# Optimization experiments

Measured on AMD Instinct MI355X. Metric: run time of the kernel, lower is better.

## Reference

```python
import jax, jax.numpy as jnp
import numpy as np
import math

B, N, C = 1, 2048, 256
H, CH = 8, 32
PQ, PV = 8, 12
CZ = 32
BQ, BK = 32, 128
NB = N // BQ
PAD = (BK - BQ) // 2
INF = 1e8
EPS = 1e-8

_KIDX = np.arange(NB)[:, None] * BQ + np.arange(BK)[None, :] - PAD
_KVALID = (_KIDX >= 0) & (_KIDX < N)
_KIDX_C = np.clip(_KIDX, 0, N - 1)


def _quat_to_rot(q):
    q = q / jnp.linalg.norm(q, axis=-1, keepdims=True)
    w, x, y, z = q[..., 0], q[..., 1], q[..., 2], q[..., 3]
    return jnp.stack([
        jnp.stack([1 - 2 * (y * y + z * z), 2 * (x * y - w * z), 2 * (x * z + w * y)], -1),
        jnp.stack([2 * (x * y + w * z), 1 - 2 * (x * x + z * z), 2 * (y * z - w * x)], -1),
        jnp.stack([2 * (x * z - w * y), 2 * (y * z + w * x), 1 - 2 * (x * x + y * y)], -1)], -2)


def _to_queries(x):
    # [B, N, ...] -> [B, NB, BQ, ...]
    return x.reshape((B, NB, BQ) + x.shape[2:])


def _to_keys(x):
    # [B, N, ...] -> [B, NB, BK, ...] zero-padded sliding key windows
    g = x[:, _KIDX_C]
    v = jnp.asarray(_KVALID, x.dtype).reshape((1, NB, BK) + (1,) * (x.ndim - 2))
    return g * v


def _ln(x):
    m = x.mean(-1, keepdims=True)
    var = x.var(-1, keepdims=True)
    return (x - m) / jnp.sqrt(var + 1e-5)


def setup_inputs():
    key = jax.random.key(0)
    ks = jax.random.split(key, 16)
    p = 0.02
    return {
        's': jax.random.normal(ks[0], (B, N, C), jnp.float32),
        'cond': jax.random.normal(ks[1], (B, N, C), jnp.float32),
        'z': jax.random.normal(ks[2], (B, NB, BQ, BK, CZ), jnp.float32),
        'trans': jax.random.normal(ks[3], (B, N, 3), jnp.float32),
        'rots': _quat_to_rot(jax.random.normal(ks[4], (B, N, 4), jnp.float32)),
        's_mask': jnp.ones((B, N), jnp.float32),
        'Wq': jax.random.normal(ks[5], (C, H * CH)) * p,
        'Wk': jax.random.normal(ks[6], (C, H * CH)) * p,
        'Wv': jax.random.normal(ks[7], (C, H * CH)) * p,
        'Wqp': jax.random.normal(ks[8], (C, H * PQ * 3)) * p,
        'Wkvp': jax.random.normal(ks[9], (C, H * (PQ + PV) * 3)) * p,
        'Wb': jax.random.normal(ks[10], (CZ, H)) * p,
        'Wdz': jax.random.normal(ks[11], (CZ, CZ // 4)) * p,
        'head_weights': jnp.full((H,), 0.5413),
        'Wout': jax.random.normal(ks[12], (H * (CZ // 4 + CH + PV * 4), C)) * p,
        'Wg': jax.random.normal(ks[13], (C, C)) * p,
        'bg': jnp.zeros((C,)),
        'Wbeta': jax.random.normal(ks[14], (C, C)) * p,
        'bbeta': jnp.zeros((C,)),
        'g_z': jnp.ones((CZ,)),
        'b_z': jnp.zeros((CZ,)),
    }


def reference(s, cond, z, trans, rots, s_mask, Wq, Wk, Wv, Wqp, Wkvp, Wb, Wdz,
              head_weights, Wout, Wg, bg, Wbeta, bbeta, g_z, b_z):
    # AdaLN on s conditioned on cond; LayerNorm on z
    s = _ln(s) * (cond @ Wg + bg) + (cond @ Wbeta + bbeta)
    z = _ln(z) * g_z + b_z

    q_in = _to_queries(s)            # [B,NB,BQ,C]
    k_in = _to_keys(s)               # [B,NB,BK,C]
    q_t = _to_queries(trans)         # [B,NB,BQ,3]
    q_R = _to_queries(rots)          # [B,NB,BQ,3,3]
    k_t = _to_keys(trans)
    k_R = _to_keys(rots)
    # zero-padded key rotations -> identity
    zero = jnp.all(k_R == 0, axis=(-2, -1))[..., None, None]
    k_R = jnp.where(zero, jnp.eye(3, dtype=k_R.dtype), k_R)

    q = (q_in @ Wq).reshape(B, NB, BQ, H, CH)
    k = (k_in @ Wk).reshape(B, NB, BK, H, CH)
    v = (k_in @ Wv).reshape(B, NB, BK, H, CH)

    q_pts = (q_in @ Wqp).reshape(B, NB, BQ, H * PQ, 3)
    q_pts = jnp.einsum('bnqij,bnqpj->bnqpi', q_R, q_pts) + q_t[..., None, :]
    q_pts = q_pts.reshape(B, NB, BQ, H, PQ, 3)

    kv_pts = (k_in @ Wkvp).reshape(B, NB, BK, H * (PQ + PV), 3)
    kv_pts = jnp.einsum('bnkij,bnkpj->bnkpi', k_R, kv_pts) + k_t[..., None, :]
    kv_pts = kv_pts.reshape(B, NB, BK, H, PQ + PV, 3)
    k_pts, v_pts = kv_pts[..., :PQ, :], kv_pts[..., PQ:, :]

    b = z @ Wb                                    # [B,NB,BQ,BK,H]
    a = jnp.einsum('bnqhc,bnkhc->bnqkh', q, k) * math.sqrt(1.0 / (3 * CH))
    a = a + math.sqrt(1.0 / 3.0) * b

    disp = q_pts[:, :, :, None] - k_pts[:, :, None]   # [B,NB,BQ,BK,H,PQ,3]
    d2 = jnp.sum(disp * disp, axis=-1)                # [B,NB,BQ,BK,H,PQ]
    hw = jax.nn.softplus(head_weights) * math.sqrt(1.0 / (3 * (PQ * 9.0 / 2)))
    pt_att = -0.5 * jnp.sum(d2 * hw[:, None], axis=-1)   # [B,NB,BQ,BK,H]

    m_q = _to_queries(s_mask[..., None])              # [B,NB,BQ,1]
    m_k = _to_keys(s_mask[..., None])                 # [B,NB,BK,1]
    attn_mask = m_q * jnp.swapaxes(m_k, -1, -2)       # [B,NB,BQ,BK]
    attn_mask = INF * (attn_mask - 1.0)

    a = a + pt_att + attn_mask[..., None]
    a = jnp.swapaxes(a, -1, -2)                       # [B,NB,BQ,H,BK]
    a = jax.nn.softmax(a, axis=-1)

    o = jnp.einsum('bnqhk,bnkhc->bnqhc', a, v).reshape(B, NB, BQ, H * CH)
    o_pt = jnp.einsum('bnqhk,bnkhvc->bnqhvc', a, v_pts)      # [B,NB,BQ,H,PV,3]
    o_pt = jnp.einsum('bnqji,bnqhvj->bnqhvi', q_R,
                      o_pt - q_t[:, :, :, None, None, :])     # invert apply
    o_pt_norm = jnp.sqrt(jnp.sum(o_pt ** 2, -1) + EPS).reshape(B, NB, BQ, H * PV)
    o_pt = o_pt.reshape(B, NB, BQ, H * PV * 3)
    pair_z = z @ Wdz                                          # [B,NB,BQ,BK,CZ//4]
    o_pair = jnp.einsum('bnqhk,bnqkc->bnqhc', a, pair_z).reshape(B, NB, BQ, H * (CZ // 4))

    out = jnp.concatenate([o, o_pt, o_pt_norm, o_pair], -1) @ Wout
    return out.reshape(B, N, C)
```

## Files before the change

### kernel.cpp

```cpp
#include <hip/hip_runtime.h>
#include <hip/hip_bf16.h>
#include <math.h>

typedef __hip_bfloat16 bf16;
typedef __attribute__((ext_vector_type(8))) short short8;
typedef __attribute__((ext_vector_type(4))) float f32x4;

#define NRES 2048
#define CDIM 256
#define PADK 48
#define POS 1440

static __device__ __forceinline__ float b2f(bf16 x) { return __bfloat162float(x); }

static __device__ __forceinline__ bool flag_f32(const void* smask) {
    return *(const unsigned int*)smask == 0x3F800000u;
}
static __device__ __forceinline__ float dual_load(const void* p, size_t i, bool f32) {
    float vf = ((const float*)p)[f32 ? i : 0];
    float vb = b2f(((const bf16*)p)[f32 ? (size_t)0 : i]);
    return f32 ? vf : vb;
}

struct TransTable {
    const void* src[8];
    bf16* dst[8];
    int srcN[8];
    int nOff[8];
    int dstStride[8];
    int tileOff[9];
};
__global__ __launch_bounds__(256) void k_trans(TransTable tb, const void* __restrict__ smask) {
    bool f32 = flag_f32(smask);
    int b = blockIdx.x;
    int s = 0;
    while (b >= tb.tileOff[s + 1]) ++s;
    int rel = b - tb.tileOff[s];
    int ntTiles = tb.srcN[s] >> 5;
    int kt = rel / ntTiles, nt = rel % ntTiles;
    const void* src = tb.src[s];
    int srcN = tb.srcN[s];
    __shared__ float tile[32][33];
    int tx = threadIdx.x & 31, ty = threadIdx.x >> 5;
#pragma unroll
    for (int r = 0; r < 4; ++r) {
        int srow = kt * 32 + ty + r * 8;
        int scol = nt * 32 + tx;
        tile[ty + r * 8][tx] = dual_load(src, (size_t)srow * srcN + scol, f32);
    }
    __syncthreads();
    bf16* dst = tb.dst[s];
#pragma unroll
    for (int r = 0; r < 4; ++r) {
        int n = nt * 32 + ty + r * 8 + tb.nOff[s];
        int k = kt * 32 + tx;
        dst[(size_t)n * tb.dstStride[s] + k] = __float2bfloat16(tile[tx][ty + r * 8]);
    }
}

__global__ __launch_bounds__(256) void k_cast(const void* __restrict__ src, bf16* __restrict__ dst,
                                              int n, const void* __restrict__ smask) {
    bool f32 = flag_f32(smask);
    for (int i = blockIdx.x * 256 + threadIdx.x; i < n; i += gridDim.x * 256)
        dst[i] = __float2bfloat16(dual_load(src, i, f32));
}

__global__ __launch_bounds__(256) void k_gemm(
    const bf16* __restrict__ A, const bf16* __restrict__ Bt, void* __restrict__ Cv,
    int M, int N, int K, int totalTiles, int out_mode, const void* __restrict__ smask)
{
    int wid = threadIdx.x >> 6, lane = threadIdx.x & 63;
    int tid = blockIdx.x * 4 + wid;
    if (tid >= totalTiles) return;
    int tiles_n = N >> 4;
    int mt = tid / tiles_n, nt = tid % tiles_n;
    int idx = lane & 15, quad = lane >> 4;
    const bf16* Ap = A + (size_t)(mt * 16 + idx) * K + quad * 8;
    const bf16* Bp = Bt + (size_t)(nt * 16 + idx) * K + quad * 8;
    f32x4 acc = {0.f, 0.f, 0.f, 0.f};
    for (int k = 0; k < K; k += 32) {
        short8 af = *(const short8*)(Ap + k);
        short8 bfv = *(const short8*)(Bp + k);
        acc = __builtin_amdgcn_mfma_f32_16x16x32_bf16(af, bfv, acc, 0, 0, 0);
    }
    int orow = mt * 16 + quad * 4;
    int ocol = nt * 16 + idx;
    if (out_mode == 0) {
        float* C = (float*)Cv;
#pragma unroll
        for (int r = 0; r < 4; ++r) C[(size_t)(orow + r) * N + ocol] = acc[r];
    } else {
        if (flag_f32(smask)) {
            float* C = (float*)Cv;
#pragma unroll
            for (int r = 0; r < 4; ++r) C[(size_t)(orow + r) * N + ocol] = acc[r];
        } else {
            bf16* C = (bf16*)Cv;
#pragma unroll
            for (int r = 0; r < 4; ++r) C[(size_t)(orow + r) * N + ocol] = __float2bfloat16(acc[r]);
        }
    }
}

__global__ __launch_bounds__(256) void k_gemm22(
    const bf16* __restrict__ A, const bf16* __restrict__ Bt, float* __restrict__ C,
    int N, int K, int totalWaves)
{
    int wid = threadIdx.x >> 6, lane = threadIdx.x & 63;
    int tid = blockIdx.x * 4 + wid;
    if (tid >= totalWaves) return;
    int tiles_n = N >> 5;
    int mt = tid / tiles_n, nt = tid % tiles_n;
    int idx = lane & 15, quad = lane >> 4;
    const bf16* Ap0 = A + (size_t)(mt * 32 + idx) * K + quad * 8;
    const bf16* Ap1 = Ap0 + (size_t)16 * K;
    const bf16* Bp0 = Bt + (size_t)(nt * 32 + idx) * K + quad * 8;
    const bf16* Bp1 = Bp0 + (size_t)16 * K;
    f32x4 a00 = {0,0,0,0}, a01 = {0,0,0,0}, a10 = {0,0,0,0}, a11 = {0,0,0,0};
    for (int k = 0; k < K; k += 32) {
        short8 af0 = *(const short8*)(Ap0 + k);
        short8 af1 = *(const short8*)(Ap1 + k);
        short8 bf0 = *(const short8*)(Bp0 + k);
        short8 bf1 = *(const short8*)(Bp1 + k);
        a00 = __builtin_amdgcn_mfma_f32_16x16x32_bf16(af0, bf0, a00, 0, 0, 0);
        a01 = __builtin_amdgcn_mfma_f32_16x16x32_bf16(af0, bf1, a01, 0, 0, 0);
        a10 = __builtin_amdgcn_mfma_f32_16x16x32_bf16(af1, bf0, a10, 0, 0, 0);
        a11 = __builtin_amdgcn_mfma_f32_16x16x32_bf16(af1, bf1, a11, 0, 0, 0);
    }
    int orow = mt * 32 + quad * 4;
    int ocol = nt * 32 + idx;
#pragma unroll
    for (int r = 0; r < 4; ++r) {
        C[(size_t)(orow + r) * N + ocol] = a00[r];
        C[(size_t)(orow + r) * N + ocol + 16] = a01[r];
        C[(size_t)(orow + r + 16) * N + ocol] = a10[r];
        C[(size_t)(orow + r + 16) * N + ocol + 16] = a11[r];
    }
}

__global__ __launch_bounds__(256) void k_mod2(
    const void* __restrict__ s, const float* __restrict__ GB,
    const void* __restrict__ bg, const void* __restrict__ bbeta,
    const void* __restrict__ smask, bf16* __restrict__ SQb)
{
    __shared__ float ls[8][CDIM];
    __shared__ float mrs[8][2];
    bool f32 = flag_f32(smask);
    int r0 = blockIdx.x * 8;
    int t = threadIdx.x;
    for (int i = t; i < 8 * CDIM; i += 256) {
        int r = i >> 8, c = i & 255;
        ls[r][c] = dual_load(s, (size_t)(r0 + r) * CDIM + c, f32);
    }
    __syncthreads();
    int wave = t >> 6, lane = t & 63;
    for (int rr = 0; rr < 2; ++rr) {
        int r = wave * 2 + rr;
        float sum = 0.f, sq = 0.f;
        for (int j = lane; j < CDIM; j += 64) { float v = ls[r][j]; sum += v; sq += v * v; }
        for (int off = 32; off; off >>= 1) { sum += __shfl_xor(sum, off); sq += __shfl_xor(sq, off); }
        if (lane == 0) {
            float m = sum / CDIM;
            float var = fmaxf(sq / CDIM - m * m, 0.f);
            mrs[r][0] = m; mrs[r][1] = rsqrtf(var + 1e-5f);
        }
    }
    __syncthreads();
    int c = t;
    float bgc = dual_load(bg, c, f32), bbc = dual_load(bbeta, c, f32);
#pragma unroll
    for (int r = 0; r < 8; ++r) {
        float xn = (ls[r][c] - mrs[r][0]) * mrs[r][1];
        float gv = GB[(size_t)(r0 + r) * 512 + c] + bgc;
        float bv = GB[(size_t)(r0 + r) * 512 + 256 + c] + bbc;
        SQb[(size_t)(r0 + r) * CDIM + c] = __float2bfloat16(xn * gv + bv);
    }
}

__global__ __launch_bounds__(256) void k_rotate(
    const float* __restrict__ PO,
    const void* __restrict__ rots, const void* __restrict__ trans,
    const void* __restrict__ smask,
    float* __restrict__ QP, float* __restrict__ KP, float* __restrict__ VP)
{
    int i = blockIdx.x;
    int t = threadIdx.x;
    bool f32 = flag_f32(smask);
    __shared__ float R[9], T[3];
    if (t < 9) R[t] = dual_load(rots, (size_t)i * 9 + t, f32);
    if (t < 3) T[t] = dual_load(trans, (size_t)i * 3 + t, f32);
    __syncthreads();
    const float* qp = PO + (size_t)i * POS + 768;
    const float* kvp = PO + (size_t)i * POS + 960;
    if (t < 64) {
        int p = t;
        float x = qp[p * 3 + 0], y = qp[p * 3 + 1], z = qp[p * 3 + 2];
#pragma unroll
        for (int d = 0; d < 3; ++d)
            QP[(size_t)i * 192 + p * 3 + d] = R[d * 3] * x + R[d * 3 + 1] * y + R[d * 3 + 2] * z + T[d];
    } else if (t < 224) {
        int pp = t - 64;
        int h = pp / 20, j = pp % 20;
        float x = kvp[pp * 3 + 0], y = kvp[pp * 3 + 1], z = kvp[pp * 3 + 2];
        float o[3];
#pragma unroll
        for (int d = 0; d < 3; ++d)
            o[d] = R[d * 3] * x + R[d * 3 + 1] * y + R[d * 3 + 2] * z + T[d];
        if (j < 8) {
#pragma unroll
            for (int d = 0; d < 3; ++d) KP[(size_t)i * 192 + (h * 8 + j) * 3 + d] = o[d];
        } else {
#pragma unroll
            for (int d = 0; d < 3; ++d) VP[(size_t)i * 288 + (h * 12 + (j - 8)) * 3 + d] = o[d];
        }
    }
}

__global__ __launch_bounds__(256) void k_z(
    const void* __restrict__ z, const void* __restrict__ Wb, const void* __restrict__ Wdz,
    const void* __restrict__ g_z, const void* __restrict__ b_z,
    const void* __restrict__ smask,
    float* __restrict__ Bz, float* __restrict__ PZ)
{
    __shared__ float wb[32][8], wdz[32][8], gz[32], bz[32];
    bool f32 = flag_f32(smask);
    int t = threadIdx.x;
    {
        int j = t >> 3, c = t & 7;
        wb[j][c] = dual_load(Wb, t, f32);
        wdz[j][c] = dual_load(Wdz, t, f32);
    }
    if (t < 32) { gz[t] = dual_load(g_z, t, f32); bz[t] = dual_load(b_z, t, f32); }
    __syncthreads();
    size_t r = (size_t)blockIdx.x * 256 + t;
    float zv[32];
    float sum = 0.f, sq = 0.f;
    if (f32) {
        const float4* zp = (const float4*)((const float*)z + r * 32);
#pragma unroll
        for (int j4 = 0; j4 < 8; ++j4) {
            float4 v4 = zp[j4];
            zv[j4 * 4 + 0] = v4.x; zv[j4 * 4 + 1] = v4.y; zv[j4 * 4 + 2] = v4.z; zv[j4 * 4 + 3] = v4.w;
        }
    } else {
        const bf16* zp = (const bf16*)z + r * 32;
#pragma unroll
        for (int j = 0; j < 32; ++j) zv[j] = b2f(zp[j]);
    }
#pragma unroll
    for (int j = 0; j < 32; ++j) { float v = zv[j]; sum += v; sq += v * v; }
    float m = sum / 32.f;
    float var = fmaxf(sq / 32.f - m * m, 0.f);
    float rstd = rsqrtf(var + 1e-5f);
#pragma unroll
    for (int j = 0; j < 32; ++j) zv[j] = (zv[j] - m) * rstd * gz[j] + bz[j];
    float bacc[8], pacc[8];
#pragma unroll
    for (int c = 0; c < 8; ++c) { bacc[c] = 0.f; pacc[c] = 0.f; }
    for (int j = 0; j < 32; ++j) {
        float v = zv[j];
#pragma unroll
        for (int c = 0; c < 8; ++c) { bacc[c] += v * wb[j][c]; pacc[c] += v * wdz[j][c]; }
    }
    int n = (int)(r >> 12);
    int q = (int)(r >> 7) & 31;
    int k = (int)r & 127;
#pragma unroll
    for (int h = 0; h < 8; ++h)
        Bz[(size_t)n * 32768 + (size_t)h * 4096 + q * 128 + k] = bacc[h];
#pragma unroll
    for (int c = 0; c < 8; ++c)
        PZ[(((size_t)(n * 32 + q)) * 8 + c) * 128 + k] = pacc[c];
}

__global__ __launch_bounds__(256) void k_attn_out(
    const float* __restrict__ PO,
    const float* __restrict__ QP, const float* __restrict__ KP, const float* __restrict__ VP,
    const float* __restrict__ Bz, const float* __restrict__ PZ,
    const void* __restrict__ rots, const void* __restrict__ trans,
    const void* __restrict__ smask, const void* __restrict__ head_weights,
    bf16* __restrict__ CATb)
{
    __shared__ char buf[70016];
    __shared__ float rowq[32], rowk[128], mk[128], mqv[32];
    bf16* Qf  = (bf16*)buf;
    bf16* Kf  = (bf16*)(buf + 4608);
    bf16* Vt  = (bf16*)(buf + 23040);
    bf16* As  = (bf16*)(buf + 44800);
    float* S  = (float*)(buf + 53504);
    float* OPT = (float*)(buf + 53504);

    const int n = blockIdx.x >> 3, h = blockIdx.x & 7;
    const int t = threadIdx.x;
    const bool f32 = flag_f32(smask);
    const int n32 = n * 32;

    float hwv = dual_load(head_weights, h, f32);
    float ptc = -0.5f * log1pf(expf(hwv)) * 0.09622504486493764f;
    float m2ptc = -2.f * ptc;
    const float qkscale = 0.10206207261596575f;
    const float bscale = 0.5773502691896258f;

    for (int i = t; i < 32 * 16; i += 256) {
        int q = i >> 4, g = i & 15;
        float4 v = {0.f, 0.f, 0.f, 0.f};
        int col;
        if (g < 8) { v = *(const float4*)(PO + (size_t)(n32 + q) * POS + h * 32 + g * 4); col = g * 4; }
        else if (g < 14) { v = *(const float4*)(QP + (size_t)(n32 + q) * 192 + h * 24 + (g - 8) * 4); col = 32 + (g - 8) * 4; }
        else col = 56 + (g - 14) * 4;
        bf16* wp = Qf + q * 72 + col;
        wp[0] = __float2bfloat16(v.x); wp[1] = __float2bfloat16(v.y);
        wp[2] = __float2bfloat16(v.z); wp[3] = __float2bfloat16(v.w);
    }
    for (int i = t; i < 128 * 16; i += 256) {
        int k = i >> 4, g = i & 15;
        int kg = n32 + k - PADK;
        bool valid = (kg >= 0 && kg < NRES);
        float4 v = {0.f, 0.f, 0.f, 0.f};
        int col;
        if (g < 8) {
            if (valid) {
                v = *(const float4*)(PO + (size_t)kg * POS + 256 + h * 32 + g * 4);
                v.x *= qkscale; v.y *= qkscale; v.z *= qkscale; v.w *= qkscale;
            }
            col = g * 4;
        } else if (g < 14) {
            if (valid) {
                v = *(const float4*)(KP + (size_t)kg * 192 + h * 24 + (g - 8) * 4);
                v.x *= m2ptc; v.y *= m2ptc; v.z *= m2ptc; v.w *= m2ptc;
            }
            col = 32 + (g - 8) * 4;
        } else col = 56 + (g - 14) * 4;
        bf16* wp = Kf + k * 72 + col;
        wp[0] = __float2bfloat16(v.x); wp[1] = __float2bfloat16(v.y);
        wp[2] = __float2bfloat16(v.z); wp[3] = __float2bfloat16(v.w);
    }
    for (int i = t; i < 128 * 17; i += 256) {
        int k = i / 17, g = i % 17;
        int kg = n32 + k - PADK;
        bool valid = (kg >= 0 && kg < NRES);
        float4 v = {0.f, 0.f, 0.f, 0.f};
        int x0;
        if (g < 8) {
            if (valid) v = *(const float4*)(PO + (size_t)kg * POS + 512 + h * 32 + g * 4);
            x0 = g * 4;
        } else {
            if (valid) v = *(const float4*)(VP + (size_t)kg * 288 + h * 36 + (g - 8) * 4);
            x0 = 32 + (g - 8) * 4;
        }
        Vt[(x0 + 0) * 136 + k] = __float2bfloat16(v.x);
        Vt[(x0 + 1) * 136 + k] = __float2bfloat16(v.y);
        Vt[(x0 + 2) * 136 + k] = __float2bfloat16(v.z);
        Vt[(x0 + 3) * 136 + k] = __float2bfloat16(v.w);
    }
    for (int i = t; i < 12 * 128; i += 256) {
        int x = 68 + (i >> 7), k = i & 127;
        Vt[x * 136 + k] = __float2bfloat16(0.f);
    }
    if (t < 32) {
        mqv[t] = dual_load(smask, n32 + t, f32);
        float s2 = 0.f;
#pragma unroll
        for (int j = 0; j < 24; ++j) {
            float v = QP[(size_t)(n32 + t) * 192 + h * 24 + j];
            s2 += v * v;
        }
        rowq[t] = ptc * s2;
    }
    if (t >= 128) {
        int k = t - 128;
        int kg = n32 + k - PADK;
        bool valid = (kg >= 0 && kg < NRES);
        float mv = 0.f, s2 = 0.f;
        if (valid) {
            mv = dual_load(smask, kg, f32);
#pragma unroll
            for (int j = 0; j < 24; ++j) {
                float v = KP[(size_t)kg * 192 + h * 24 + j];
                s2 += v * v;
            }
        }
        mk[k] = mv;
        rowk[k] = ptc * s2;
    }
    __syncthreads();

    const int wid = t >> 6, lane = t & 63, idx = lane & 15, quad = lane >> 4;
#pragma unroll
    for (int i = 0; i < 4; ++i) {
        int tt = wid * 4 + i;
        int mt = tt >> 3, nt = tt & 7;
        f32x4 acc = {0.f, 0.f, 0.f, 0.f};
#pragma unroll
        for (int kk = 0; kk < 2; ++kk) {
            short8 af  = *(const short8*)(Qf + (mt * 16 + idx) * 72 + kk * 32 + quad * 8);
            short8 bfv = *(const short8*)(Kf + (nt * 16 + idx) * 72 + kk * 32 + quad * 8);
            acc = __builtin_amdgcn_mfma_f32_16x16x32_bf16(af, bfv, acc, 0, 0, 0);
        }
#pragma unroll
        for (int r = 0; r < 4; ++r) {
            int q = mt * 16 + quad * 4 + r;
            int k = nt * 16 + idx;
            float bz = Bz[(size_t)n * 32768 + (size_t)h * 4096 + q * 128 + k];
            float msk = 1e8f * (mqv[q] * mk[k] - 1.f);
            S[q * 129 + k] = acc[r] + bscale * bz + rowq[q] + rowk[k] + msk;
        }
    }
    __syncthreads();

    for (int rr = 0; rr < 8; ++rr) {
        int q = wid * 8 + rr;
        float v0 = S[q * 129 + lane], v1 = S[q * 129 + lane + 64];
        float mx = fmaxf(v0, v1);
        for (int off = 32; off; off >>= 1) mx = fmaxf(mx, __shfl_xor(mx, off));
        float e0 = expf(v0 - mx), e1 = expf(v1 - mx);
        float sm = e0 + e1;
        for (int off = 32; off; off >>= 1) sm += __shfl_xor(sm, off);
        float inv = 1.f / sm;
        As[q * 136 + lane] = __float2bfloat16(e0 * inv);
        As[q * 136 + lane + 64] = __float2bfloat16(e1 * inv);
    }
    __syncthreads();

    {
        int q = t >> 3, c = t & 7;
        const float4* pzp = (const float4*)(PZ + (((size_t)(n32 + q)) * 8 + c) * 128);
        float acc = 0.f;
        for (int k4 = 0; k4 < 32; ++k4) {
            float4 pv = pzp[k4];
            int k = k4 * 4;
            acc += b2f(As[q * 136 + k + 0]) * pv.x + b2f(As[q * 136 + k + 1]) * pv.y
                 + b2f(As[q * 136 + k + 2]) * pv.z + b2f(As[q * 136 + k + 3]) * pv.w;
        }
        CATb[(size_t)(n32 + q) * 704 + 640 + h * 8 + c] = __float2bfloat16(acc);
    }
#pragma unroll
    for (int i = 0; i < 3; ++i) {
        int tt = wid + i * 4;
        if (tt >= 10) break;
        int mt = tt / 5, nt = tt % 5;
        f32x4 acc = {0.f, 0.f, 0.f, 0.f};
#pragma unroll
        for (int kk = 0; kk < 4; ++kk) {
            short8 af  = *(const short8*)(As + (mt * 16 + idx) * 136 + kk * 32 + quad * 8);
            short8 bfv = *(const short8*)(Vt + (nt * 16 + idx) * 136 + kk * 32 + quad * 8);
            acc = __builtin_amdgcn_mfma_f32_16x16x32_bf16(af, bfv, acc, 0, 0, 0);
        }
        int x = nt * 16 + idx;
#pragma unroll
        for (int r = 0; r < 4; ++r) {
            int q = mt * 16 + quad * 4 + r;
            if (x < 32)
                CATb[(size_t)(n32 + q) * 704 + h * 32 + x] = __float2bfloat16(acc[r]);
            else if (x < 68)
                OPT[q * 37 + (x - 32)] = acc[r];
        }
    }
    __syncthreads();

    for (int i = t; i < 32 * 12; i += 256) {
        int q = i / 12, v = i % 12;
        int g = n32 + q;
        float R[9], T[3];
#pragma unroll
        for (int d = 0; d < 9; ++d) R[d] = dual_load(rots, (size_t)g * 9 + d, f32);
#pragma unroll
        for (int d = 0; d < 3; ++d) T[d] = dual_load(trans, (size_t)g * 3 + d, f32);
        float x = OPT[q * 37 + v * 3 + 0] - T[0];
        float y = OPT[q * 37 + v * 3 + 1] - T[1];
        float z = OPT[q * 37 + v * 3 + 2] - T[2];
        float o0 = R[0] * x + R[3] * y + R[6] * z;
        float o1 = R[1] * x + R[4] * y + R[7] * z;
        float o2 = R[2] * x + R[5] * y + R[8] * z;
        size_t cb = (size_t)g * 704;
        CATb[cb + 256 + (h * 12 + v) * 3 + 0] = __float2bfloat16(o0);
        CATb[cb + 256 + (h * 12 + v) * 3 + 1] = __float2bfloat16(o1);
        CATb[cb + 256 + (h * 12 + v) * 3 + 2] = __float2bfloat16(o2);
        CATb[cb + 544 + h * 12 + v] = __float2bfloat16(sqrtf(o0 * o0 + o1 * o1 + o2 * o2 + 1e-8f));
    }
}

extern "C" void kernel_launch(void* const* d_in, const int* in_sizes, int n_in,
                              void* d_out, int out_size, void* d_ws, size_t ws_size,
                              hipStream_t stream) {
    const void* s       = d_in[0];
    const void* cond    = d_in[1];
    const void* z       = d_in[2];
    const void* trans   = d_in[3];
    const void* rots    = d_in[4];
    const void* s_mask  = d_in[5];
    const void* Wq      = d_in[6];
    const void* Wk      = d_in[7];
    const void* Wv      = d_in[8];
    const void* Wqp     = d_in[9];
    const void* Wkvp    = d_in[10];
    const void* Wb      = d_in[11];
    const void* Wdz     = d_in[12];
    const void* hweights= d_in[13];
    const void* Wout    = d_in[14];
    const void* Wg      = d_in[15];
    const void* bg      = d_in[16];
    const void* Wbeta   = d_in[17];
    const void* bbeta   = d_in[18];
    const void* g_z     = d_in[19];
    const void* b_z     = d_in[20];

    float* ws = (float*)d_ws;
    float* PO   = ws;
    float* GB   = PO + 2949120;
    float* QP   = GB + 1048576;
    float* KP   = QP + 393216;
    float* VP   = KP + 393216;
    float* Bz   = VP + 589824;
    float* PZ   = Bz + 2097152;
    float* fb   = PZ + 2097152;
    bf16* SQb   = (bf16*)fb;
    bf16* condb = (bf16*)(fb + 262144);
    bf16* CATb  = (bf16*)(fb + 524288);
    bf16* PWt   = (bf16*)(fb + 1245184);
    bf16* GWt   = (bf16*)(fb + 1429504);
    bf16* FWt   = (bf16*)(fb + 1495040);

    TransTable tb;
    tb.src[0] = Wq;   tb.dst[0] = PWt; tb.srcN[0] = 256; tb.nOff[0] = 0;   tb.dstStride[0] = 256;
    tb.src[1] = Wk;   tb.dst[1] = PWt; tb.srcN[1] = 256; tb.nOff[1] = 256; tb.dstStride[1] = 256;
    tb.src[2] = Wv;   tb.dst[2] = PWt; tb.srcN[2] = 256; tb.nOff[2] = 512; tb.dstStride[2] = 256;
    tb.src[3] = Wqp;  tb.dst[3] = PWt; tb.srcN[3] = 192; tb.nOff[3] = 768; tb.dstStride[3] = 256;
    tb.src[4] = Wkvp; tb.dst[4] = PWt; tb.srcN[4] = 480; tb.nOff[4] = 960; tb.dstStride[4] = 256;
    tb.src[5] = Wg;   tb.dst[5] = GWt; tb.srcN[5] = 256; tb.nOff[5] = 0;   tb.dstStride[5] = 256;
    tb.src[6] = Wbeta;tb.dst[6] = GWt; tb.srcN[6] = 256; tb.nOff[6] = 256; tb.dstStride[6] = 256;
    tb.src[7] = Wout; tb.dst[7] = FWt; tb.srcN[7] = 256; tb.nOff[7] = 0;   tb.dstStride[7] = 704;
    int tc[8] = {64, 64, 64, 48, 120, 64, 64, 176};
    tb.tileOff[0] = 0;
    for (int i = 0; i < 8; ++i) tb.tileOff[i + 1] = tb.tileOff[i] + tc[i];

    dim3 blk(256);
    k_trans<<<dim3(664), blk, 0, stream>>>(tb, s_mask);
    k_cast<<<dim3(256), blk, 0, stream>>>(cond, condb, NRES * CDIM, s_mask);
    k_gemm<<<dim3(1024), blk, 0, stream>>>(condb, GWt, GB, 2048, 512, 256, 4096, 0, s_mask);
    k_mod2<<<dim3(256), blk, 0, stream>>>(s, GB, bg, bbeta, s_mask, SQb);
    k_gemm22<<<dim3(720), blk, 0, stream>>>(SQb, PWt, PO, 1440, 256, 2880);
    k_rotate<<<dim3(NRES), blk, 0, stream>>>(PO, rots, trans, s_mask, QP, KP, VP);
    k_z<<<dim3(1024), blk, 0, stream>>>(z, Wb, Wdz, g_z, b_z, s_mask, Bz, PZ);
    k_attn_out<<<dim3(512), blk, 0, stream>>>(PO, QP, KP, VP, Bz, PZ, rots, trans, s_mask, hweights, CATb);
    k_gemm<<<dim3(512), blk, 0, stream>>>(CATb, FWt, d_out, 2048, 256, 704, 2048, 1, s_mask);
}
```

Measured before the change: 199.7 us.

## Fuse prep kernels, fold scales into weights, and store intermediates as bf16

Merges the weight transposes, the cond cast and the s layernorm into one prep launch. It fuses the gamma/beta GEMM with the modulation epilogue, and folds the qk and bias scales into the weights. The projection output and the pair-bias/pair-z intermediates are now stored as bf16, and the separate rotate kernel is removed so points are handled inside attention. This cuts the launch count and halves intermediate memory traffic, at the cost of extra bf16 rounding on intermediates.

```diff
diff --git a/kernel.cpp b/kernel.cpp
--- a/kernel.cpp
+++ b/kernel.cpp
@@ -12,7 +12,13 @@
 #define POS 1440
 
 static __device__ __forceinline__ float b2f(bf16 x) { return __bfloat162float(x); }
-
+static __device__ __forceinline__ float us2f(short u) {
+    return __uint_as_float(((unsigned)(unsigned short)u) << 16);
+}
+static __device__ __forceinline__ short f2s(float f) {
+    bf16 h = __float2bfloat16(f);
+    return *reinterpret_cast<short*>(&h);
+}
 static __device__ __forceinline__ bool flag_f32(const void* smask) {
     return *(const unsigned int*)smask == 0x3F800000u;
 }
@@ -22,88 +28,117 @@
     return f32 ? vf : vb;
 }
 
-struct TransTable {
+struct PrepTable {
     const void* src[8];
     bf16* dst[8];
     int srcN[8];
     int nOff[8];
     int dstStride[8];
+    float scl[8];
     int tileOff[9];
+    const void* s;
+    const void* cond;
+    bf16* condb;
+    bf16* xnb;
 };
-__global__ __launch_bounds__(256) void k_trans(TransTable tb, const void* __restrict__ smask) {
+__global__ __launch_bounds__(256) void k_prep(PrepTable tb, const void* __restrict__ smask) {
     bool f32 = flag_f32(smask);
     int b = blockIdx.x;
-    int s = 0;
-    while (b >= tb.tileOff[s + 1]) ++s;
-    int rel = b - tb.tileOff[s];
-    int ntTiles = tb.srcN[s] >> 5;
-    int kt = rel / ntTiles, nt = rel % ntTiles;
-    const void* src = tb.src[s];
-    int srcN = tb.srcN[s];
-    __shared__ float tile[32][33];
-    int tx = threadIdx.x & 31, ty = threadIdx.x >> 5;
-#pragma unroll
-    for (int r = 0; r < 4; ++r) {
-        int srow = kt * 32 + ty + r * 8;
-        int scol = nt * 32 + tx;
-        tile[ty + r * 8][tx] = dual_load(src, (size_t)srow * srcN + scol, f32);
-    }
-    __syncthreads();
-    bf16* dst = tb.dst[s];
-#pragma unroll
-    for (int r = 0; r < 4; ++r) {
-        int n = nt * 32 + ty + r * 8 + tb.nOff[s];
-        int k = kt * 32 + tx;
-        dst[(size_t)n * tb.dstStride[s] + k] = __float2bfloat16(tile[tx][ty + r * 8]);
-    }
-}
-
-__global__ __launch_bounds__(256) void k_cast(const void* __restrict__ src, bf16* __restrict__ dst,
-                                              int n, const void* __restrict__ smask) {
+    int t = threadIdx.x;
+    if (b < tb.tileOff[8]) {
+        int s = 0;
+        while (b >= tb.tileOff[s + 1]) ++s;
+        int rel = b - tb.tileOff[s];
+        int ntTiles = tb.srcN[s] >> 5;
+        int kt = rel / ntTiles, nt = rel % ntTiles;
+        const void* src = tb.src[s];
+        int srcN = tb.srcN[s];
+        float scl = tb.scl[s];
+        __shared__ float tile[32][33];
+        int tx = t & 31, ty = t >> 5;
+#pragma unroll
+        for (int r = 0; r < 4; ++r) {
+            int srow = kt * 32 + ty + r * 8;
+            int scol = nt * 32 + tx;
+            tile[ty + r * 8][tx] = dual_load(src, (size_t)srow * srcN + scol, f32);
+        }
+        __syncthreads();
+        bf16* dst = tb.dst[s];
+#pragma unroll
+        for (int r = 0; r < 4; ++r) {
+            int n = nt * 32 + ty + r * 8 + tb.nOff[s];
+            int k = kt * 32 + tx;
+            dst[(size_t)n * tb.dstStride[s] + k] = __float2bfloat16(tile[tx][ty + r * 8] * scl);
+        }
+        return;
+    }
+    b -= tb.tileOff[8];
+    if (b < 256) {
+        int i0 = b * 2048;
+        for (int i = t; i < 2048; i += 256)
+            tb.condb[i0 + i] = __float2bfloat16(dual_load(tb.cond, (size_t)(i0 + i), f32));
+        return;
+    }
+    b -= 256;
+    __shared__ float ls[8][CDIM];
+    __shared__ float mrs[8][2];
+    int r0 = b * 8;
+    for (int i = t; i < 8 * CDIM; i += 256) {
+        int r = i >> 8, c = i & 255;
+        ls[r][c] = dual_load(tb.s, (size_t)(r0 + r) * CDIM + c, f32);
+    }
+    __syncthreads();
+    int wave = t >> 6, lane = t & 63;
+    for (int rr = 0; rr < 2; ++rr) {
+        int r = wave * 2 + rr;
+        float sum = 0.f, sq = 0.f;
+        for (int j = lane; j < CDIM; j += 64) { float v = ls[r][j]; sum += v; sq += v * v; }
+        for (int off = 32; off; off >>= 1) { sum += __shfl_xor(sum, off); sq += __shfl_xor(sq, off); }
+        if (lane == 0) {
+            float m = sum / CDIM;
+            float var = fmaxf(sq / CDIM - m * m, 0.f);
+            mrs[r][0] = m; mrs[r][1] = rsqrtf(var + 1e-5f);
+        }
+    }
+    __syncthreads();
+    int c = t;
+#pragma unroll
+    for (int r = 0; r < 8; ++r)
+        tb.xnb[(size_t)(r0 + r) * CDIM + c] = __float2bfloat16((ls[r][c] - mrs[r][0]) * mrs[r][1]);
+}
+
+__global__ __launch_bounds__(256) void k_gb(
+    const bf16* __restrict__ condb, const bf16* __restrict__ GWt, const bf16* __restrict__ xnb,
+    const void* __restrict__ bg, const void* __restrict__ bbeta,
+    const void* __restrict__ smask, bf16* __restrict__ SQb)
+{
     bool f32 = flag_f32(smask);
-    for (int i = blockIdx.x * 256 + threadIdx.x; i < n; i += gridDim.x * 256)
-        dst[i] = __float2bfloat16(dual_load(src, i, f32));
-}
-
-__global__ __launch_bounds__(256) void k_gemm(
-    const bf16* __restrict__ A, const bf16* __restrict__ Bt, void* __restrict__ Cv,
-    int M, int N, int K, int totalTiles, int out_mode, const void* __restrict__ smask)
-{
     int wid = threadIdx.x >> 6, lane = threadIdx.x & 63;
     int tid = blockIdx.x * 4 + wid;
-    if (tid >= totalTiles) return;
-    int tiles_n = N >> 4;
-    int mt = tid / tiles_n, nt = tid % tiles_n;
+    int mt = tid >> 4, nt = tid & 15;
     int idx = lane & 15, quad = lane >> 4;
-    const bf16* Ap = A + (size_t)(mt * 16 + idx) * K + quad * 8;
-    const bf16* Bp = Bt + (size_t)(nt * 16 + idx) * K + quad * 8;
-    f32x4 acc = {0.f, 0.f, 0.f, 0.f};
-    for (int k = 0; k < K; k += 32) {
+    const bf16* Ap = condb + (size_t)(mt * 16 + idx) * 256 + quad * 8;
+    const bf16* B0 = GWt + (size_t)(nt * 16 + idx) * 256 + quad * 8;
+    const bf16* B1 = GWt + (size_t)(256 + nt * 16 + idx) * 256 + quad * 8;
+    f32x4 a0 = {0,0,0,0}, a1 = {0,0,0,0};
+    for (int k = 0; k < 256; k += 32) {
         short8 af = *(const short8*)(Ap + k);
-        short8 bfv = *(const short8*)(Bp + k);
-        acc = __builtin_amdgcn_mfma_f32_16x16x32_bf16(af, bfv, acc, 0, 0, 0);
-    }
+        a0 = __builtin_amdgcn_mfma_f32_16x16x32_bf16(af, *(const short8*)(B0 + k), a0, 0, 0, 0);
+        a1 = __builtin_amdgcn_mfma_f32_16x16x32_bf16(af, *(const short8*)(B1 + k), a1, 0, 0, 0);
+    }
+    int ocol = nt * 16 + idx;
+    float bgc = dual_load(bg, ocol, f32), bbc = dual_load(bbeta, ocol, f32);
     int orow = mt * 16 + quad * 4;
-    int ocol = nt * 16 + idx;
-    if (out_mode == 0) {
-        float* C = (float*)Cv;
-#pragma unroll
-        for (int r = 0; r < 4; ++r) C[(size_t)(orow + r) * N + ocol] = acc[r];
-    } else {
-        if (flag_f32(smask)) {
-            float* C = (float*)Cv;
-#pragma unroll
-            for (int r = 0; r < 4; ++r) C[(size_t)(orow + r) * N + ocol] = acc[r];
-        } else {
-            bf16* C = (bf16*)Cv;
-#pragma unroll
-            for (int r = 0; r < 4; ++r) C[(size_t)(orow + r) * N + ocol] = __float2bfloat16(acc[r]);
-        }
-    }
-}
-
-__global__ __launch_bounds__(256) void k_gemm22(
-    const bf16* __restrict__ A, const bf16* __restrict__ Bt, float* __restrict__ C,
+#pragma unroll
+    for (int r = 0; r < 4; ++r) {
+        int row = orow + r;
+        float xn = b2f(xnb[(size_t)row * 256 + ocol]);
+        SQb[(size_t)row * 256 + ocol] = __float2bfloat16(xn * (a0[r] + bgc) + (a1[r] + bbc));
+    }
+}
+
+__global__ __launch_bounds__(256) void k_gemm22b(
+    const bf16* __restrict__ A, const bf16* __restrict__ Bt, bf16* __restrict__ C,
     int N, int K, int totalWaves)
 {
     int wid = threadIdx.x >> 6, lane = threadIdx.x & 63;
@@ -131,88 +166,10 @@
     int ocol = nt * 32 + idx;
 #pragma unroll
     for (int r = 0; r < 4; ++r) {
-        C[(size_t)(orow + r) * N + ocol] = a00[r];
-        C[(size_t)(orow + r) * N + ocol + 16] = a01[r];
-        C[(size_t)(orow + r + 16) * N + ocol] = a10[r];
-        C[(size_t)(orow + r + 16) * N + ocol + 16] = a11[r];
-    }
-}
-
-__global__ __launch_bounds__(256) void k_mod2(
-    const void* __restrict__ s, const float* __restrict__ GB,
-    const void* __restrict__ bg, const void* __restrict__ bbeta,
-    const void* __restrict__ smask, bf16* __restrict__ SQb)
-{
-    __shared__ float ls[8][CDIM];
-    __shared__ float mrs[8][2];
-    bool f32 = flag_f32(smask);
-    int r0 = blockIdx.x * 8;
-    int t = threadIdx.x;
-    for (int i = t; i < 8 * CDIM; i += 256) {
-        int r = i >> 8, c = i & 255;
-        ls[r][c] = dual_load(s, (size_t)(r0 + r) * CDIM + c, f32);
-    }
-    __syncthreads();
-    int wave = t >> 6, lane = t & 63;
-    for (int rr = 0; rr < 2; ++rr) {
-        int r = wave * 2 + rr;
-        float sum = 0.f, sq = 0.f;
-        for (int j = lane; j < CDIM; j += 64) { float v = ls[r][j]; sum += v; sq += v * v; }
-        for (int off = 32; off; off >>= 1) { sum += __shfl_xor(sum, off); sq += __shfl_xor(sq, off); }
-        if (lane == 0) {
-            float m = sum / CDIM;
-            float var = fmaxf(sq / CDIM - m * m, 0.f);
-            mrs[r][0] = m; mrs[r][1] = rsqrtf(var + 1e-5f);
-        }
-    }
-    __syncthreads();
-    int c = t;
-    float bgc = dual_load(bg, c, f32), bbc = dual_load(bbeta, c, f32);
-#pragma unroll
-    for (int r = 0; r < 8; ++r) {
-        float xn = (ls[r][c] - mrs[r][0]) * mrs[r][1];
-        float gv = GB[(size_t)(r0 + r) * 512 + c] + bgc;
-        float bv = GB[(size_t)(r0 + r) * 512 + 256 + c] + bbc;
-        SQb[(size_t)(r0 + r) * CDIM + c] = __float2bfloat16(xn * gv + bv);
-    }
-}
-
-__global__ __launch_bounds__(256) void k_rotate(
-    const float* __restrict__ PO,
-    const void* __restrict__ rots, const void* __restrict__ trans,
-    const void* __restrict__ smask,
-    float* __restrict__ QP, float* __restrict__ KP, float* __restrict__ VP)
-{
-    int i = blockIdx.x;
-    int t = threadIdx.x;
-    bool f32 = flag_f32(smask);
-    __shared__ float R[9], T[3];
-    if (t < 9) R[t] = dual_load(rots, (size_t)i * 9 + t, f32);
-    if (t < 3) T[t] = dual_load(trans, (size_t)i * 3 + t, f32);
-    __syncthreads();
-    const float* qp = PO + (size_t)i * POS + 768;
-    const float* kvp = PO + (size_t)i * POS + 960;
-    if (t < 64) {
-        int p = t;
-        float x = qp[p * 3 + 0], y = qp[p * 3 + 1], z = qp[p * 3 + 2];
-#pragma unroll
-        for (int d = 0; d < 3; ++d)
-            QP[(size_t)i * 192 + p * 3 + d] = R[d * 3] * x + R[d * 3 + 1] * y + R[d * 3 + 2] * z + T[d];
-    } else if (t < 224) {
-        int pp = t - 64;
-        int h = pp / 20, j = pp % 20;
-        float x = kvp[pp * 3 + 0], y = kvp[pp * 3 + 1], z = kvp[pp * 3 + 2];
-        float o[3];
-#pragma unroll
-        for (int d = 0; d < 3; ++d)
-            o[d] = R[d * 3] * x + R[d * 3 + 1] * y + R[d * 3 + 2] * z + T[d];
-        if (j < 8) {
-#pragma unroll
-            for (int d = 0; d < 3; ++d) KP[(size_t)i * 192 + (h * 8 + j) * 3 + d] = o[d];
-        } else {
-#pragma unroll
-            for (int d = 0; d < 3; ++d) VP[(size_t)i * 288 + (h * 12 + (j - 8)) * 3 + d] = o[d];
-        }
+        C[(size_t)(orow + r) * N + ocol] = __float2bfloat16(a00[r]);
+        C[(size_t)(orow + r) * N + ocol + 16] = __float2bfloat16(a01[r]);
+        C[(size_t)(orow + r + 16) * N + ocol] = __float2bfloat16(a10[r]);
+        C[(size_t)(orow + r + 16) * N + ocol + 16] = __float2bfloat16(a11[r]);
     }
 }
 
@@ -220,14 +177,14 @@
     const void* __restrict__ z, const void* __restrict__ Wb, const void* __restrict__ Wdz,
     const void* __restrict__ g_z, const void* __restrict__ b_z,
     const void* __restrict__ smask,
-    float* __restrict__ Bz, float* __restrict__ PZ)
+    bf16* __restrict__ Bzb, bf16* __restrict__ PZb)
 {
     __shared__ float wb[32][8], wdz[32][8], gz[32], bz[32];
     bool f32 = flag_f32(smask);
     int t = threadIdx.x;
     {
         int j = t >> 3, c = t & 7;
-        wb[j][c] = dual_load(Wb, t, f32);
+        wb[j][c] = 0.5773502691896258f * dual_load(Wb, t, f32);
         wdz[j][c] = dual_load(Wdz, t, f32);
     }
     if (t < 32) { gz[t] = dual_load(g_z, t, f32); bz[t] = dual_load(b_z, t, f32); }
@@ -267,27 +224,26 @@
     int k = (int)r & 127;
 #pragma unroll
     for (int h = 0; h < 8; ++h)
-        Bz[(size_t)n * 32768 + (size_t)h * 4096 + q * 128 + k] = bacc[h];
+        Bzb[(size_t)n * 32768 + (size_t)h * 4096 + q * 128 + k] = __float2bfloat16(bacc[h]);
 #pragma unroll
     for (int c = 0; c < 8; ++c)
-        PZ[(((size_t)(n * 32 + q)) * 8 + c) * 128 + k] = pacc[c];
+        PZb[(((size_t)(n * 32 + q)) * 8 + c) * 128 + k] = __float2bfloat16(pacc[c]);
 }
 
 __global__ __launch_bounds__(256) void k_attn_out(
-    const float* __restrict__ PO,
-    const float* __restrict__ QP, const float* __restrict__ KP, const float* __restrict__ VP,
-    const float* __restrict__ Bz, const float* __restrict__ PZ,
+    const bf16* __restrict__ POb,
+    const bf16* __restrict__ Bzb, const bf16* __restrict__ PZb,
     const void* __restrict__ rots, const void* __restrict__ trans,
     const void* __restrict__ smask, const void* __restrict__ head_weights,
     bf16* __restrict__ CATb)
 {
     __shared__ char buf[70016];
     __shared__ float rowq[32], rowk[128], mk[128], mqv[32];
-    bf16* Qf  = (bf16*)buf;
-    bf16* Kf  = (bf16*)(buf + 4608);
-    bf16* Vt  = (bf16*)(buf + 23040);
-    bf16* As  = (bf16*)(buf + 44800);
-    float* S  = (float*)(buf + 53504);
+    short* QfS = (short*)buf;
+    short* KfS = (short*)(buf + 4608);
+    short* VtS = (short*)(buf + 23040);
+    short* AsS = (short*)(buf + 44800);
+    float* S   = (float*)(buf + 53504);
     float* OPT = (float*)(buf + 53504);
 
     const int n = blockIdx.x >> 3, h = blockIdx.x & 7;
@@ -298,90 +254,98 @@
     float hwv = dual_load(head_weights, h, f32);
     float ptc = -0.5f * log1pf(expf(hwv)) * 0.09622504486493764f;
     float m2ptc = -2.f * ptc;
-    const float qkscale = 0.10206207261596575f;
-    const float bscale = 0.5773502691896258f;
-
-    for (int i = t; i < 32 * 16; i += 256) {
-        int q = i >> 4, g = i & 15;
-        float4 v = {0.f, 0.f, 0.f, 0.f};
-        int col;
-        if (g < 8) { v = *(const float4*)(PO + (size_t)(n32 + q) * POS + h * 32 + g * 4); col = g * 4; }
-        else if (g < 14) { v = *(const float4*)(QP + (size_t)(n32 + q) * 192 + h * 24 + (g - 8) * 4); col = 32 + (g - 8) * 4; }
-        else col = 56 + (g - 14) * 4;
-        bf16* wp = Qf + q * 72 + col;
-        wp[0] = __float2bfloat16(v.x); wp[1] = __float2bfloat16(v.y);
-        wp[2] = __float2bfloat16(v.z); wp[3] = __float2bfloat16(v.w);
-    }
-    for (int i = t; i < 128 * 16; i += 256) {
-        int k = i >> 4, g = i & 15;
+    const short8 zero8 = {0,0,0,0,0,0,0,0};
+
+    if (t < 128) {
+        int q = t >> 2, g = t & 3;
+        *(short8*)(QfS + q * 72 + g * 8) =
+            *(const short8*)(POb + (size_t)(n32 + q) * POS + h * 32 + g * 8);
+    }
+    for (int i = t; i < 512; i += 256) {
+        int k = i >> 2, g = i & 3;
         int kg = n32 + k - PADK;
-        bool valid = (kg >= 0 && kg < NRES);
-        float4 v = {0.f, 0.f, 0.f, 0.f};
-        int col;
-        if (g < 8) {
-            if (valid) {
-                v = *(const float4*)(PO + (size_t)kg * POS + 256 + h * 32 + g * 4);
-                v.x *= qkscale; v.y *= qkscale; v.z *= qkscale; v.w *= qkscale;
-            }
-            col = g * 4;
-        } else if (g < 14) {
-            if (valid) {
-                v = *(const float4*)(KP + (size_t)kg * 192 + h * 24 + (g - 8) * 4);
-                v.x *= m2ptc; v.y *= m2ptc; v.z *= m2ptc; v.w *= m2ptc;
-            }
-            col = 32 + (g - 8) * 4;
-        } else col = 56 + (g - 14) * 4;
-        bf16* wp = Kf + k * 72 + col;
-        wp[0] = __float2bfloat16(v.x); wp[1] = __float2bfloat16(v.y);
-        wp[2] = __float2bfloat16(v.z); wp[3] = __float2bfloat16(v.w);
-    }
-    for (int i = t; i < 128 * 17; i += 256) {
-        int k = i / 17, g = i % 17;
+        short8 v = zero8;
+        if (kg >= 0 && kg < NRES)
+            v = *(const short8*)(POb + (size_t)kg * POS + 256 + h * 32 + g * 8);
+        *(short8*)(KfS + k * 72 + g * 8) = v;
+    }
+    for (int i = t; i < 512; i += 256) {
+        int k = i >> 2, g = i & 3;
         int kg = n32 + k - PADK;
-        bool valid = (kg >= 0 && kg < NRES);
-        float4 v = {0.f, 0.f, 0.f, 0.f};
-        int x0;
-        if (g < 8) {
-            if (valid) v = *(const float4*)(PO + (size_t)kg * POS + 512 + h * 32 + g * 4);
-            x0 = g * 4;
-        } else {
-            if (valid) v = *(const float4*)(VP + (size_t)kg * 288 + h * 36 + (g - 8) * 4);
-            x0 = 32 + (g - 8) * 4;
-        }
-        Vt[(x0 + 0) * 136 + k] = __float2bfloat16(v.x);
-        Vt[(x0 + 1) * 136 + k] = __float2bfloat16(v.y);
-        Vt[(x0 + 2) * 136 + k] = __float2bfloat16(v.z);
-        Vt[(x0 + 3) * 136 + k] = __float2bfloat16(v.w);
-    }
-    for (int i = t; i < 12 * 128; i += 256) {
-        int x = 68 + (i >> 7), k = i & 127;
-        Vt[x * 136 + k] = __float2bfloat16(0.f);
-    }
-    if (t < 32) {
-        mqv[t] = dual_load(smask, n32 + t, f32);
-        float s2 = 0.f;
-#pragma unroll
-        for (int j = 0; j < 24; ++j) {
-            float v = QP[(size_t)(n32 + t) * 192 + h * 24 + j];
-            s2 += v * v;
-        }
-        rowq[t] = ptc * s2;
-    }
-    if (t >= 128) {
-        int k = t - 128;
+        short8 v = zero8;
+        if (kg >= 0 && kg < NRES)
+            v = *(const short8*)(POb + (size_t)kg * POS + 512 + h * 32 + g * 8);
+#pragma unroll
+        for (int j = 0; j < 8; ++j) VtS[(g * 8 + j) * 136 + k] = v[j];
+    }
+    for (int i = t; i < 320; i += 256) {
+        if (i < 64) { int q = i >> 1, g = i & 1; *(short8*)(QfS + q * 72 + 56 + g * 8) = zero8; }
+        else { int j = i - 64; int k = j >> 1, g = j & 1; *(short8*)(KfS + k * 72 + 56 + g * 8) = zero8; }
+    }
+    for (int i = t; i < 204; i += 256) {
+        int r = 68 + i / 17, sg = i % 17;
+        *(short8*)(VtS + r * 136 + sg * 8) = zero8;
+    }
+    if (t >= 64 && t < 192) {
+        int k = t - 64;
         int kg = n32 + k - PADK;
         bool valid = (kg >= 0 && kg < NRES);
         float mv = 0.f, s2 = 0.f;
         if (valid) {
+            float R[9], T[3];
+#pragma unroll
+            for (int d = 0; d < 9; ++d) R[d] = dual_load(rots, (size_t)kg * 9 + d, f32);
+#pragma unroll
+            for (int d = 0; d < 3; ++d) T[d] = dual_load(trans, (size_t)kg * 3 + d, f32);
             mv = dual_load(smask, kg, f32);
-#pragma unroll
-            for (int j = 0; j < 24; ++j) {
-                float v = KP[(size_t)kg * 192 + h * 24 + j];
-                s2 += v * v;
+            const bf16* kv = POb + (size_t)kg * POS + 960 + h * 60;
+#pragma unroll
+            for (int j = 0; j < 20; ++j) {
+                float x = b2f(kv[j * 3]), y = b2f(kv[j * 3 + 1]), z = b2f(kv[j * 3 + 2]);
+                float p0 = R[0] * x + R[1] * y + R[2] * z + T[0];
+                float p1 = R[3] * x + R[4] * y + R[5] * z + T[1];
+                float p2 = R[6] * x + R[7] * y + R[8] * z + T[2];
+                if (j < 8) {
+                    KfS[k * 72 + 32 + j * 3 + 0] = f2s(p0);
+                    KfS[k * 72 + 32 + j * 3 + 1] = f2s(p1);
+                    KfS[k * 72 + 32 + j * 3 + 2] = f2s(p2);
+                    s2 += p0 * p0 + p1 * p1 + p2 * p2;
+                } else {
+                    int v = j - 8;
+                    VtS[(32 + v * 3 + 0) * 136 + k] = f2s(p0);
+                    VtS[(32 + v * 3 + 1) * 136 + k] = f2s(p1);
+                    VtS[(32 + v * 3 + 2) * 136 + k] = f2s(p2);
+                }
             }
-        }
+        } else {
+            for (int c = 32; c < 56; ++c) KfS[k * 72 + c] = 0;
+            for (int x = 32; x < 68; ++x) VtS[x * 136 + k] = 0;
+        }
+        rowk[k] = ptc * s2;
         mk[k] = mv;
-        rowk[k] = ptc * s2;
+    } else if (t >= 224) {
+        int q = t - 224;
+        int g = n32 + q;
+        float R[9], T[3];
+#pragma unroll
+        for (int d = 0; d < 9; ++d) R[d] = dual_load(rots, (size_t)g * 9 + d, f32);
+#pragma unroll
+        for (int d = 0; d < 3; ++d) T[d] = dual_load(trans, (size_t)g * 3 + d, f32);
+        mqv[q] = dual_load(smask, g, f32);
+        const bf16* qv = POb + (size_t)g * POS + 768 + h * 24;
+        float s2 = 0.f;
+#pragma unroll
+        for (int p = 0; p < 8; ++p) {
+            float x = b2f(qv[p * 3]), y = b2f(qv[p * 3 + 1]), z = b2f(qv[p * 3 + 2]);
+            float p0 = R[0] * x + R[1] * y + R[2] * z + T[0];
+            float p1 = R[3] * x + R[4] * y + R[5] * z + T[1];
+            float p2 = R[6] * x + R[7] * y + R[8] * z + T[2];
+            QfS[q * 72 + 32 + p * 3 + 0] = f2s(m2ptc * p0);
+            QfS[q * 72 + 32 + p * 3 + 1] = f2s(m2ptc * p1);
+            QfS[q * 72 + 32 + p * 3 + 2] = f2s(m2ptc * p2);
+            s2 += p0 * p0 + p1 * p1 + p2 * p2;
+        }
+        rowq[q] = ptc * s2;
     }
     __syncthreads();
 
@@ -393,17 +357,17 @@
         f32x4 acc = {0.f, 0.f, 0.f, 0.f};
 #pragma unroll
         for (int kk = 0; kk < 2; ++kk) {
-            short8 af  = *(const short8*)(Qf + (mt * 16 + idx) * 72 + kk * 32 + quad * 8);
-            short8 bfv = *(const short8*)(Kf + (nt * 16 + idx) * 72 + kk * 32 + quad * 8);
+            short8 af  = *(const short8*)(QfS + (mt * 16 + idx) * 72 + kk * 32 + quad * 8);
+            short8 bfv = *(const short8*)(KfS + (nt * 16 + idx) * 72 + kk * 32 + quad * 8);
             acc = __builtin_amdgcn_mfma_f32_16x16x32_bf16(af, bfv, acc, 0, 0, 0);
         }
 #pragma unroll
         for (int r = 0; r < 4; ++r) {
             int q = mt * 16 + quad * 4 + r;
             int k = nt * 16 + idx;
-            float bz = Bz[(size_t)n * 32768 + (size_t)h * 4096 + q * 128 + k];
+            float bz = b2f(Bzb[(size_t)n * 32768 + (size_t)h * 4096 + q * 128 + k]);
             float msk = 1e8f * (mqv[q] * mk[k] - 1.f);
-            S[q * 129 + k] = acc[r] + bscale * bz + rowq[q] + rowk[k] + msk;
+            S[q * 129 + k] = acc[r] + bz + rowq[q] + rowk[k] + msk;
         }
     }
     __syncthreads();
@@ -417,20 +381,21 @@
         float sm = e0 + e1;
         for (int off = 32; off; off >>= 1) sm += __shfl_xor(sm, off);
         float inv = 1.f / sm;
-        As[q * 136 + lane] = __float2bfloat16(e0 * inv);
-        As[q * 136 + lane + 64] = __float2bfloat16(e1 * inv);
+        AsS[q * 136 + lane] = f2s(e0 * inv);
+        AsS[q * 136 + lane + 64] = f2s(e1 * inv);
     }
     __syncthreads();
 
     {
         int q = t >> 3, c = t & 7;
-        const float4* pzp = (const float4*)(PZ + (((size_t)(n32 + q)) * 8 + c) * 128);
+        const short8* pzp = (const short8*)(PZb + ((size_t)(n32 + q) * 8 + c) * 128);
+        const short8* asp = (const short8*)(AsS + q * 136);
         float acc = 0.f;
-        for (int k4 = 0; k4 < 32; ++k4) {
-            float4 pv = pzp[k4];
-            int k = k4 * 4;
-            acc += b2f(As[q * 136 + k + 0]) * pv.x + b2f(As[q * 136 + k + 1]) * pv.y
-                 + b2f(As[q * 136 + k + 2]) * pv.z + b2f(As[q * 136 + k + 3]) * pv.w;
+        for (int k8 = 0; k8 < 16; ++k8) {
+            short8 pv = pzp[k8];
+            short8 av = asp[k8];
+#pragma unroll
+            for (int j = 0; j < 8; ++j) acc += us2f(av[j]) * us2f(pv[j]);
         }
         CATb[(size_t)(n32 + q) * 704 + 640 + h * 8 + c] = __float2bfloat16(acc);
     }
@@ -442,8 +407,8 @@
         f32x4 acc = {0.f, 0.f, 0.f, 0.f};
 #pragma unroll
         for (int kk = 0; kk < 4; ++kk) {
-            short8 af  = *(const short8*)(As + (mt * 16 + idx) * 136 + kk * 32 + quad * 8);
-            short8 bfv = *(const short8*)(Vt + (nt * 16 + idx) * 136 + kk * 32 + quad * 8);
+            short8 af  = *(const short8*)(AsS + (mt * 16 + idx) * 136 + kk * 32 + quad * 8);
+            short8 bfv = *(const short8*)(VtS + (nt * 16 + idx) * 136 + kk * 32 + quad * 8);
             acc = __builtin_amdgcn_mfma_f32_16x16x32_bf16(af, bfv, acc, 0, 0, 0);
         }
         int x = nt * 16 + idx;
@@ -477,6 +442,37 @@
         CATb[cb + 256 + (h * 12 + v) * 3 + 1] = __float2bfloat16(o1);
         CATb[cb + 256 + (h * 12 + v) * 3 + 2] = __float2bfloat16(o2);
         CATb[cb + 544 + h * 12 + v] = __float2bfloat16(sqrtf(o0 * o0 + o1 * o1 + o2 * o2 + 1e-8f));
+    }
+}
+
+__global__ __launch_bounds__(256) void k_gemm(
+    const bf16* __restrict__ A, const bf16* __restrict__ Bt, void* __restrict__ Cv,
+    int N, int K, int totalTiles, const void* __restrict__ smask)
+{
+    int wid = threadIdx.x >> 6, lane = threadIdx.x & 63;
+    int tid = blockIdx.x * 4 + wid;
+    if (tid >= totalTiles) return;
+    int tiles_n = N >> 4;
+    int mt = tid / tiles_n, nt = tid % tiles_n;
+    int idx = lane & 15, quad = lane >> 4;
+    const bf16* Ap = A + (size_t)(mt * 16 + idx) * K + quad * 8;
+    const bf16* Bp = Bt + (size_t)(nt * 16 + idx) * K + quad * 8;
+    f32x4 acc = {0.f, 0.f, 0.f, 0.f};
+    for (int k = 0; k < K; k += 32) {
+        short8 af = *(const short8*)(Ap + k);
+        short8 bfv = *(const short8*)(Bp + k);
+        acc = __builtin_amdgcn_mfma_f32_16x16x32_bf16(af, bfv, acc, 0, 0, 0);
+    }
+    int orow = mt * 16 + quad * 4;
+    int ocol = nt * 16 + idx;
+    if (flag_f32(smask)) {
+        float* C = (float*)Cv;
+#pragma unroll
+        for (int r = 0; r < 4; ++r) C[(size_t)(orow + r) * N + ocol] = acc[r];
+    } else {
+        bf16* C = (bf16*)Cv;
+#pragma unroll
+        for (int r = 0; r < 4; ++r) C[(size_t)(orow + r) * N + ocol] = __float2bfloat16(acc[r]);
     }
 }
 
@@ -506,42 +502,37 @@
     const void* b_z     = d_in[20];
 
     float* ws = (float*)d_ws;
-    float* PO   = ws;
-    float* GB   = PO + 2949120;
-    float* QP   = GB + 1048576;
-    float* KP   = QP + 393216;
-    float* VP   = KP + 393216;
-    float* Bz   = VP + 589824;
-    float* PZ   = Bz + 2097152;
-    float* fb   = PZ + 2097152;
-    bf16* SQb   = (bf16*)fb;
-    bf16* condb = (bf16*)(fb + 262144);
-    bf16* CATb  = (bf16*)(fb + 524288);
-    bf16* PWt   = (bf16*)(fb + 1245184);
-    bf16* GWt   = (bf16*)(fb + 1429504);
-    bf16* FWt   = (bf16*)(fb + 1495040);
-
-    TransTable tb;
-    tb.src[0] = Wq;   tb.dst[0] = PWt; tb.srcN[0] = 256; tb.nOff[0] = 0;   tb.dstStride[0] = 256;
-    tb.src[1] = Wk;   tb.dst[1] = PWt; tb.srcN[1] = 256; tb.nOff[1] = 256; tb.dstStride[1] = 256;
-    tb.src[2] = Wv;   tb.dst[2] = PWt; tb.srcN[2] = 256; tb.nOff[2] = 512; tb.dstStride[2] = 256;
-    tb.src[3] = Wqp;  tb.dst[3] = PWt; tb.srcN[3] = 192; tb.nOff[3] = 768; tb.dstStride[3] = 256;
-    tb.src[4] = Wkvp; tb.dst[4] = PWt; tb.srcN[4] = 480; tb.nOff[4] = 960; tb.dstStride[4] = 256;
-    tb.src[5] = Wg;   tb.dst[5] = GWt; tb.srcN[5] = 256; tb.nOff[5] = 0;   tb.dstStride[5] = 256;
-    tb.src[6] = Wbeta;tb.dst[6] = GWt; tb.srcN[6] = 256; tb.nOff[6] = 256; tb.dstStride[6] = 256;
-    tb.src[7] = Wout; tb.dst[7] = FWt; tb.srcN[7] = 256; tb.nOff[7] = 0;   tb.dstStride[7] = 704;
+    bf16* POb   = (bf16*)(ws);
+    bf16* Bzb   = (bf16*)(ws + 1474560);
+    bf16* PZb   = (bf16*)(ws + 2523136);
+    bf16* SQb   = (bf16*)(ws + 3571712);
+    bf16* condb = (bf16*)(ws + 3833856);
+    bf16* xnb   = (bf16*)(ws + 4096000);
+    bf16* CATb  = (bf16*)(ws + 4358144);
+    bf16* PWt   = (bf16*)(ws + 5079040);
+    bf16* GWt   = (bf16*)(ws + 5263360);
+    bf16* FWt   = (bf16*)(ws + 5328896);
+
+    PrepTable tb;
+    const float qkscale = 0.10206207261596575f;
+    tb.src[0] = Wq;   tb.dst[0] = PWt; tb.srcN[0] = 256; tb.nOff[0] = 0;   tb.dstStride[0] = 256; tb.scl[0] = qkscale;
+    tb.src[1] = Wk;   tb.dst[1] = PWt; tb.srcN[1] = 256; tb.nOff[1] = 256; tb.dstStride[1] = 256; tb.scl[1] = 1.f;
+    tb.src[2] = Wv;   tb.dst[2] = PWt; tb.srcN[2] = 256; tb.nOff[2] = 512; tb.dstStride[2] = 256; tb.scl[2] = 1.f;
+    tb.src[3] = Wqp;  tb.dst[3] = PWt; tb.srcN[3] = 192; tb.nOff[3] = 768; tb.dstStride[3] = 256; tb.scl[3] = 1.f;
+    tb.src[4] = Wkvp; tb.dst[4] = PWt; tb.srcN[4] = 480; tb.nOff[4] = 960; tb.dstStride[4] = 256; tb.scl[4] = 1.f;
+    tb.src[5] = Wg;   tb.dst[5] = GWt; tb.srcN[5] = 256; tb.nOff[5] = 0;   tb.dstStride[5] = 256; tb.scl[5] = 1.f;
+    tb.src[6] = Wbeta;tb.dst[6] = GWt; tb.srcN[6] = 256; tb.nOff[6] = 256; tb.dstStride[6] = 256; tb.scl[6] = 1.f;
+    tb.src[7] = Wout; tb.dst[7] = FWt; tb.srcN[7] = 256; tb.nOff[7] = 0;   tb.dstStride[7] = 704; tb.scl[7] = 1.f;
     int tc[8] = {64, 64, 64, 48, 120, 64, 64, 176};
     tb.tileOff[0] = 0;
     for (int i = 0; i < 8; ++i) tb.tileOff[i + 1] = tb.tileOff[i] + tc[i];
+    tb.s = s; tb.cond = cond; tb.condb = condb; tb.xnb = xnb;
 
     dim3 blk(256);
-    k_trans<<<dim3(664), blk, 0, stream>>>(tb, s_mask);
-    k_cast<<<dim3(256), blk, 0, stream>>>(cond, condb, NRES * CDIM, s_mask);
-    k_gemm<<<dim3(1024), blk, 0, stream>>>(condb, GWt, GB, 2048, 512, 256, 4096, 0, s_mask);
-    k_mod2<<<dim3(256), blk, 0, stream>>>(s, GB, bg, bbeta, s_mask, SQb);
-    k_gemm22<<<dim3(720), blk, 0, stream>>>(SQb, PWt, PO, 1440, 256, 2880);
-    k_rotate<<<dim3(NRES), blk, 0, stream>>>(PO, rots, trans, s_mask, QP, KP, VP);
-    k_z<<<dim3(1024), blk, 0, stream>>>(z, Wb, Wdz, g_z, b_z, s_mask, Bz, PZ);
-    k_attn_out<<<dim3(512), blk, 0, stream>>>(PO, QP, KP, VP, Bz, PZ, rots, trans, s_mask, hweights, CATb);
-    k_gemm<<<dim3(512), blk, 0, stream>>>(CATb, FWt, d_out, 2048, 256, 704, 2048, 1, s_mask);
-}
+    k_prep<<<dim3(664 + 256 + 256), blk, 0, stream>>>(tb, s_mask);
+    k_gb<<<dim3(512), blk, 0, stream>>>(condb, GWt, xnb, bg, bbeta, s_mask, SQb);
+    k_gemm22b<<<dim3(720), blk, 0, stream>>>(SQb, PWt, POb, 1440, 256, 2880);
+    k_z<<<dim3(1024), blk, 0, stream>>>(z, Wb, Wdz, g_z, b_z, s_mask, Bzb, PZb);
+    k_attn_out<<<dim3(512), blk, 0, stream>>>(POb, Bzb, PZb, rots, trans, s_mask, hweights, CATb);
+    k_gemm<<<dim3(512), blk, 0, stream>>>(CATb, FWt, d_out, 256, 704, 2048, s_mask);
+}
```

After: 177.4 us. -11.2%, faster.
